# Performance work log

Hardware: AMD Instinct MI355X
Metric: run time of the kernel (lower is better)

The kernel has to match this reference:

```python
import jax, jax.numpy as jnp
import numpy as np

B, L = 1024, 64          # sentences, tokens per sentence
V, E = 100000, 300       # vocab, embedding dim
RH, M, NC = 50, 50, 3    # rnn_hidden, mem_dim, num_class
N = B * L                # total tree nodes


def setup_inputs() -> dict:
    key = jax.random.key(0)
    ks = jax.random.split(key, 24)
    rn = lambda k, s, sc=0.05: jax.random.normal(k, s, dtype=jnp.float32) * sc
    # balanced binary dependency tree per sentence: parent(i) = (i-1)//2
    loc = np.arange(L)
    par_loc = np.where(loc == 0, -1, (loc - 1) // 2)
    parent = np.where(par_loc[None, :] < 0, -1,
                      par_loc[None, :] + np.arange(B)[:, None] * L).reshape(-1)
    depth = np.tile(np.floor(np.log2(loc + 1)).astype(np.int64), B)
    tm = np.zeros(L, np.float32); tm[1:4] = 1.0  # 3 aspect-target tokens/sentence
    return {
        "embed_ids": jax.random.randint(ks[0], (B, L), 0, V),
        "parent": jnp.asarray(parent),
        "depth": jnp.asarray(depth),
        "target_mask": jnp.asarray(np.tile(tm, B)),
        "num_levels": 7,
        "embed_table": rn(ks[1], (V, E), 1.0),
        "W_ih_f": rn(ks[2], (4 * RH, E)), "W_hh_f": rn(ks[3], (4 * RH, RH)),
        "b_f": rn(ks[4], (4 * RH,)),
        "W_ih_b": rn(ks[5], (4 * RH, E)), "W_hh_b": rn(ks[6], (4 * RH, RH)),
        "b_b": rn(ks[7], (4 * RH,)),
        "W_iou": rn(ks[8], (3 * M, 2 * RH)),
        "U_iou_w": rn(ks[9], (3 * M, M)), "U_iou_b": rn(ks[10], (3 * M,)),
        "b_iou": jnp.zeros((3 * M,), jnp.float32),
        "U_f_w": rn(ks[11], (M, M)), "U_f_b": rn(ks[12], (M,)),
        "H_w": rn(ks[13], (M, 2 * RH)), "H_b": rn(ks[14], (M,)),
        "C_w": rn(ks[15], (NC, M)), "C_b": rn(ks[16], (NC,)),
    }


def _lstm(x, W_ih, W_hh, b, reverse):
    # x: (B, L, E) -> (B, L, H); PyTorch gate order i, f, g, o
    xg = jnp.einsum('ble,ge->blg', x, W_ih) + b
    H = W_hh.shape[1]
    def step(carry, xt):
        h, c = carry
        g = xt + h @ W_hh.T
        i, f, gg, o = jnp.split(g, 4, axis=-1)
        c = jax.nn.sigmoid(f) * c + jax.nn.sigmoid(i) * jnp.tanh(gg)
        h = jax.nn.sigmoid(o) * jnp.tanh(c)
        return (h, c), h
    z = jnp.zeros((x.shape[0], H), x.dtype)
    _, hs = jax.lax.scan(step, (z, z), jnp.swapaxes(xg, 0, 1), reverse=reverse)
    return jnp.swapaxes(hs, 0, 1)


def reference(embed_ids, parent, depth, target_mask, num_levels, embed_table,
              W_ih_f, W_hh_f, b_f, W_ih_b, W_hh_b, b_b,
              W_iou, U_iou_w, U_iou_b, b_iou, U_f_w, U_f_b,
              H_w, H_b, C_w, C_b):
    # --- BiLSTM encoder (dropout = identity at inference) ---
    emb = embed_table[embed_ids]                       # (B,L,E) gather
    hf = _lstm(emb, W_ih_f, W_hh_f, b_f, False)
    hb = _lstm(emb, W_ih_b, W_hh_b, b_b, True)
    x = jnp.concatenate([hf, hb], -1).reshape(N, 2 * RH)
    # --- ChildSum TreeLSTM, topological (deepest level first) ---
    iou0 = x @ W_iou.T                                 # (N, 3M)
    h_init = x @ H_w.T + H_b                           # (N, M)
    parent_safe = jnp.where(parent >= 0, parent, N)    # roots -> dummy slot N
    counts = jnp.zeros(N + 1, jnp.int32).at[parent_safe].add(1)
    has_children = (counts[:N] > 0)[:, None]
    h_fin = h_init
    c_fin = jnp.zeros((N, M), jnp.float32)
    h_sum = jnp.zeros((N + 1, M), jnp.float32)         # sum of child h
    fc_sum = jnp.zeros((N + 1, M), jnp.float32)        # sum of f * child c
    for lvl in range(num_levels - 1, -1, -1):
        m = (depth == lvl)[:, None]
        # reduce: leaves never get U_iou bias (no mailbox in DGL)
        iou = iou0 + jnp.where(has_children, h_sum[:N] @ U_iou_w.T + U_iou_b, 0.0) + b_iou
        i, o, u = jnp.split(iou, 3, axis=-1)
        c_new = jax.nn.sigmoid(i) * jnp.tanh(u) + fc_sum[:N]
        h_new = h_init + jax.nn.sigmoid(o) * jnp.tanh(c_new)
        h_fin = jnp.where(m, h_new, h_fin)
        c_fin = jnp.where(m, c_new, c_fin)
        # scatter messages from this level's nodes to their parents
        f = jax.nn.sigmoid(h_new @ U_f_w.T + U_f_b)
        h_sum = h_sum.at[parent_safe].add(jnp.where(m, h_new, 0.0))
        fc_sum = fc_sum.at[parent_safe].add(jnp.where(m, f * c_new, 0.0))
    # --- masked mean pool over target tokens per sentence ---
    tm = target_mask.reshape(B, L)
    pooled = (h_fin.reshape(B, L, M) * tm[:, :, None]).sum(1) / tm.sum(1, keepdims=True)
    logits = pooled @ C_w.T + C_b
    return logits, pooled
```

## Files before the change

### kernel.cpp

```cpp
#include <hip/hip_runtime.h>


typedef __attribute__((ext_vector_type(8))) short bf16x8;
typedef __attribute__((ext_vector_type(4))) float f32x4;

__device__ __forceinline__ float fsig2(float x) {
    float e = __builtin_amdgcn_exp2f(-1.4426950408889634f * x);
    return __builtin_amdgcn_rcpf(1.0f + e);
}
__device__ __forceinline__ float ftanh2(float x) {
    float e = __builtin_amdgcn_exp2f(2.8853900817779268f * x);
    return 1.0f - 2.0f * __builtin_amdgcn_rcpf(1.0f + e);
}

__device__ __forceinline__ unsigned short rne_bf16(float f) {
    unsigned u = __builtin_bit_cast(unsigned, f);
    unsigned r = u + 0x7fffu + ((u >> 16) & 1u);
    return (unsigned short)(r >> 16);
}
__device__ __forceinline__ void split2(float f, unsigned short& h, unsigned short& l) {
    h = rne_bf16(f);
    float fh = __builtin_bit_cast(float, ((unsigned)h) << 16);
    float r = f - fh;
    l = rne_bf16(r);
}

__device__ __forceinline__ void async_lds16(const void* g, void* l) {
    __builtin_amdgcn_global_load_lds(
        (const __attribute__((address_space(1))) unsigned int*)g,
        (__attribute__((address_space(3))) unsigned int*)l, 16, 0, 0);
}

__device__ __forceinline__ bf16x8 pack8(const unsigned short* h) {
    bf16x8 v;
    #pragma unroll
    for (int e = 0; e < 8; ++e) v[e] = (short)h[e];
    return v;
}

__device__ __forceinline__ void conv_item(int q, const float* __restrict__ B1,
                                          const float* __restrict__ B2,
                                          int split, int K, int Rreal, int BN,
                                          unsigned short* __restrict__ out) {
    int n  = q % BN;
    int kq = (q / BN) & 3;
    int c  = q / (BN * 4);
    const float* row = (n < split) ? (B1 + (size_t)n * K) : (B2 + (size_t)(n - split) * K);
    unsigned short h[8], l[8];
    #pragma unroll
    for (int e = 0; e < 8; ++e) {
        int k = c * 32 + kq * 8 + e;
        float v = (n < Rreal && k < K) ? row[k] : 0.0f;
        split2(v, h[e], l[e]);
    }
    size_t hb = ((((size_t)c * 2 + 0) * 4 + kq) * BN + n) * 8;
    size_t lb = ((((size_t)c * 2 + 1) * 4 + kq) * BN + n) * 8;
    *(ushort4*)&out[hb]     = make_ushort4(h[0], h[1], h[2], h[3]);
    *(ushort4*)&out[hb + 4] = make_ushort4(h[4], h[5], h[6], h[7]);
    *(ushort4*)&out[lb]     = make_ushort4(l[0], l[1], l[2], l[3]);
    *(ushort4*)&out[lb + 4] = make_ushort4(l[4], l[5], l[6], l[7]);
}

constexpr int WHC_DIR = 2 * 2 * 4 * 208 * 8;

__global__ void conv_fused(const float* __restrict__ Wihf, const float* __restrict__ Wihb,
                           const float* __restrict__ Wiou, const float* __restrict__ Hw,
                           const float* __restrict__ Whhf, const float* __restrict__ Whhb,
                           unsigned short* __restrict__ B1c,
                           unsigned short* __restrict__ B3c,
                           unsigned short* __restrict__ Whc) {
    int q = blockIdx.x * 256 + threadIdx.x;
    if (q < 17920) {
        conv_item(q, Wihf, Wihb, 200, 300, 400, 448, B1c);
    } else if (q < 22016) {
        conv_item(q - 17920, Wiou, Hw, 150, 100, 200, 256, B3c);
    } else if (q < 23680) {
        conv_item(q - 22016, Whhf, Whhf, 200, 50, 200, 208, Whc);
    } else if (q < 25344) {
        conv_item(q - 23680, Whhb, Whhb, 200, 50, 200, 208, Whc + WHC_DIR);
    }
}

template<int BN, int KCH, int KREAL, int NCOLS, bool GATHER>
__global__ __launch_bounds__(256)
void gemm_split(const float* __restrict__ A, const int* __restrict__ ids,
                const unsigned short* __restrict__ Bc,
                const float* __restrict__ bias1, const float* __restrict__ bias2,
                int split, float* __restrict__ C) {
    constexpr int NTW = BN / 64;
    __shared__ __align__(16) unsigned short As[2 * 4 * 64 * 8];
    __shared__ __align__(16) unsigned short Bt[64 * BN];

    const int tid = threadIdx.x;
    const int m0 = blockIdx.x * 64;
    const int w = tid >> 6, lane = tid & 63;
    const int r16 = lane & 15, quad = lane >> 4;
    const int wn = w * (BN / 4);

    const int mA = tid & 63, kqA = tid >> 6;
    const float* arow = GATHER ? (A + (size_t)ids[m0 + mA] * KREAL)
                               : (A + (size_t)(m0 + mA) * KREAL);

    float ar[8];
    {
        int k0 = kqA * 8;
        if (k0 + 8 <= KREAL) {
            float4 p = *(const float4*)(arow + k0);
            float4 q = *(const float4*)(arow + k0 + 4);
            ar[0]=p.x; ar[1]=p.y; ar[2]=p.z; ar[3]=p.w;
            ar[4]=q.x; ar[5]=q.y; ar[6]=q.z; ar[7]=q.w;
        } else {
            #pragma unroll
            for (int e = 0; e < 8; ++e) ar[e] = (k0 + e < KREAL) ? arow[k0 + e] : 0.0f;
        }
    }

    f32x4 acc[4][NTW] = {};

    for (int c = 0; c < KCH; ++c) {
        __syncthreads();
        {
            const unsigned short* src = Bc + (size_t)c * 64 * BN + tid * 8;
            #pragma unroll
            for (int i = 0; i < BN / 32; ++i)
                async_lds16(src + (size_t)i * 2048, Bt + i * 2048 + tid * 8);
        }
        {
            unsigned short h[8], l[8];
            #pragma unroll
            for (int e = 0; e < 8; ++e) split2(ar[e], h[e], l[e]);
            *(bf16x8*)&As[((0 * 4 + kqA) * 64 + mA) * 8] = pack8(h);
            *(bf16x8*)&As[((1 * 4 + kqA) * 64 + mA) * 8] = pack8(l);
        }
        __syncthreads();
        if (c + 1 < KCH) {
            int k0 = (c + 1) * 32 + kqA * 8;
            if (k0 + 8 <= KREAL) {
                float4 p = *(const float4*)(arow + k0);
                float4 q = *(const float4*)(arow + k0 + 4);
                ar[0]=p.x; ar[1]=p.y; ar[2]=p.z; ar[3]=p.w;
                ar[4]=q.x; ar[5]=q.y; ar[6]=q.z; ar[7]=q.w;
            } else {
                #pragma unroll
                for (int e = 0; e < 8; ++e) ar[e] = (k0 + e < KREAL) ? arow[k0 + e] : 0.0f;
            }
        }
        bf16x8 af[2][4];
        #pragma unroll
        for (int i = 0; i < 4; ++i) {
            af[0][i] = *(const bf16x8*)&As[((0 * 4 + quad) * 64 + i * 16 + r16) * 8];
            af[1][i] = *(const bf16x8*)&As[((1 * 4 + quad) * 64 + i * 16 + r16) * 8];
        }
        #pragma unroll
        for (int t = 0; t < NTW; ++t) {
            bf16x8 bh = *(const bf16x8*)&Bt[((0 * 4 + quad) * BN + wn + t * 16 + r16) * 8];
            bf16x8 bl = *(const bf16x8*)&Bt[((1 * 4 + quad) * BN + wn + t * 16 + r16) * 8];
            #pragma unroll
            for (int i = 0; i < 4; ++i) {
                acc[i][t] = __builtin_amdgcn_mfma_f32_16x16x32_bf16(af[0][i], bh, acc[i][t], 0, 0, 0);
                acc[i][t] = __builtin_amdgcn_mfma_f32_16x16x32_bf16(af[1][i], bh, acc[i][t], 0, 0, 0);
                acc[i][t] = __builtin_amdgcn_mfma_f32_16x16x32_bf16(af[0][i], bl, acc[i][t], 0, 0, 0);
            }
        }
    }

    #pragma unroll
    for (int t = 0; t < NTW; ++t) {
        int ncol = wn + t * 16 + r16;
        if (ncol < NCOLS) {
            float bv = (ncol < split) ? bias1[ncol] : bias2[ncol - split];
            #pragma unroll
            for (int i = 0; i < 4; ++i)
                #pragma unroll
                for (int r = 0; r < 4; ++r) {
                    int mrow = m0 + i * 16 + quad * 4 + r;
                    C[(size_t)mrow * NCOLS + ncol] = acc[i][t][r] + bv;
                }
        }
    }
}

__global__ __launch_bounds__(256)
void lstm_mfma(const float* __restrict__ xg, const unsigned short* __restrict__ Whc,
               float* __restrict__ x) {
    const int bi = blockIdx.x;
    const int dir = bi & 1;
    const int b0 = (bi >> 1) * 8;
    const int tid = threadIdx.x;
    const int w = tid >> 6, lane = tid & 63;
    const int r16 = lane & 15, quad = lane >> 4;

    __shared__ __align__(16) unsigned short Ah[8 * 16 * 8];
    __shared__ __align__(16) unsigned short Al[8 * 16 * 8];
    __shared__ __align__(16) float G[208 * 20];
    __shared__ __align__(16) float Xs[3][8][268];

    const int n0 = (w == 0) ? 0 : (w == 1) ? 4 : (w == 2) ? 7 : 10;
    const int nc = (w == 0) ? 4 : 3;

    const unsigned short* Wd = Whc + (size_t)dir * WHC_DIR;
    bf16x8 bfr[4][2][2];
    #pragma unroll
    for (int t = 0; t < 4; ++t) {
        int col = (n0 + ((t < nc) ? t : 0)) * 16 + r16;
        #pragma unroll
        for (int c = 0; c < 2; ++c)
            #pragma unroll
            for (int h = 0; h < 2; ++h)
                bfr[t][c][h] = *(const bf16x8*)&Wd[((((size_t)c * 2 + h) * 4 + quad) * 208 + col) * 8];
    }

    for (int q = tid; q < 512; q += 256) {
        ((unsigned*)Ah)[q] = 0u;
        ((unsigned*)Al)[q] = 0u;
    }

    int ss[2], ms[2];
    bool act[2];
    #pragma unroll
    for (int j = 0; j < 2; ++j) {
        int q = w * 100 + lane + 64 * j;
        ss[j] = q & 7;
        ms[j] = q >> 3;
        act[j] = (lane + 64 * j) < 100;
    }
    float c_reg[2] = {0.0f, 0.0f};

    #pragma unroll
    for (int p = 0; p < 2; ++p) {
        int idx0 = dir ? (63 - p) : p;
        #pragma unroll
        for (int i = 0; i < 2; ++i) {
            int s = w * 2 + i;
            const float* src = xg + ((size_t)(b0 + s) * 64 + idx0) * 400 + dir * 200 + lane * 4;
            async_lds16(src, &Xs[p][s][lane * 4]);
        }
    }
    __syncthreads();

    for (int step = 0; step < 64; ++step) {
        const int buf = step % 3;
        const int idx = dir ? (63 - step) : step;
        {
            int stepn = step + 2; if (stepn > 63) stepn = 63;
            const int slot = (step + 2) % 3;
            const int idxn = dir ? (63 - stepn) : stepn;
            #pragma unroll
            for (int i = 0; i < 2; ++i) {
                int s = w * 2 + i;
                const float* src = xg + ((size_t)(b0 + s) * 64 + idxn) * 400 + dir * 200 + lane * 4;
                async_lds16(src, &Xs[slot][s][lane * 4]);
            }
            __builtin_amdgcn_sched_barrier(0);
        }
        bf16x8 ah[2], al[2];
        #pragma unroll
        for (int c = 0; c < 2; ++c) {
            ah[c] = *(const bf16x8*)&Ah[((c * 4 + quad) * 16 + r16) * 8];
            al[c] = *(const bf16x8*)&Al[((c * 4 + quad) * 16 + r16) * 8];
        }
        f32x4 acc[4] = {};
        #pragma unroll
        for (int t = 0; t < 4; ++t) {
            if (t < nc) {
                #pragma unroll
                for (int c = 0; c < 2; ++c) {
                    acc[t] = __builtin_amdgcn_mfma_f32_16x16x32_bf16(ah[c], bfr[t][c][0], acc[t], 0, 0, 0);
                    acc[t] = __builtin_amdgcn_mfma_f32_16x16x32_bf16(al[c], bfr[t][c][0], acc[t], 0, 0, 0);
                    acc[t] = __builtin_amdgcn_mfma_f32_16x16x32_bf16(ah[c], bfr[t][c][1], acc[t], 0, 0, 0);
                }
            }
        }
        #pragma unroll
        for (int t = 0; t < 4; ++t) {
            if (t < nc) {
                int col = (n0 + t) * 16 + r16;
                *(f32x4*)&G[col * 20 + quad * 4] = acc[t];
            }
        }
        asm volatile("s_waitcnt lgkmcnt(0) vmcnt(8)" ::: "memory");
        __builtin_amdgcn_sched_barrier(0);
        __builtin_amdgcn_s_barrier();
        __builtin_amdgcn_sched_barrier(0);
        #pragma unroll
        for (int j = 0; j < 2; ++j) {
            if (act[j]) {
                int s = ss[j], m = ms[j];
                float gi = G[m * 20 + s]         + Xs[buf][s][m];
                float gf = G[(m + 50) * 20 + s]  + Xs[buf][s][m + 50];
                float gg = G[(m + 100) * 20 + s] + Xs[buf][s][m + 100];
                float go = G[(m + 150) * 20 + s] + Xs[buf][s][m + 150];
                c_reg[j] = fsig2(gf) * c_reg[j] + fsig2(gi) * ftanh2(gg);
                float h = fsig2(go) * ftanh2(c_reg[j]);
                unsigned short hh, hl;
                split2(h, hh, hl);
                Ah[(m >> 3) * 128 + s * 8 + (m & 7)] = hh;
                Al[(m >> 3) * 128 + s * 8 + (m & 7)] = hl;
                x[((size_t)(b0 + s) * 64 + idx) * 100 + dir * 50 + m] = h;
            }
        }
        asm volatile("s_waitcnt lgkmcnt(0)" ::: "memory");
        __builtin_amdgcn_sched_barrier(0);
        __builtin_amdgcn_s_barrier();
        __builtin_amdgcn_sched_barrier(0);
    }
}

__global__ __launch_bounds__(256)
void tree_kernel(const float* __restrict__ C2,
                 const float* __restrict__ Uw, const float* __restrict__ Ub,
                 const float* __restrict__ Fw, const float* __restrict__ Fb,
                 const float* __restrict__ tmask,
                 const float* __restrict__ Cw, const float* __restrict__ Cb,
                 float* __restrict__ out) {
    const int tid = threadIdx.x;
    const int w = tid >> 6, lane = tid & 63;
    const int s = blockIdx.x * 4 + w;

    __shared__ __align__(16) float Us[150][52];
    __shared__ __align__(16) float Fs[50][52];
    __shared__ __align__(16) float HS[4][32][52];
    __shared__ __align__(16) float FC[4][32][52];
    __shared__ __align__(16) float HV[4][64];
    __shared__ __align__(16) float TMS[4][64];

    for (int q = tid; q < 7500; q += 256) Us[q / 50][q % 50] = Uw[q];
    for (int q = tid; q < 2500; q += 256) Fs[q / 50][q % 50] = Fw[q];
    for (int q = tid; q < 4 * 32 * 52; q += 256) {
        int ww = q / (32 * 52), r = q - ww * (32 * 52);
        HS[ww][r / 52][r % 52] = 0.0f;
        FC[ww][r / 52][r % 52] = 0.0f;
    }
    TMS[w][lane] = tmask[(size_t)s * 64 + lane];
    __syncthreads();

    const bool act = lane < 50;
    const int m = act ? lane : 49;
    const float ub0 = Ub[m], ub1 = Ub[50 + m], ub2 = Ub[100 + m];
    const float fb = Fb[m];
    const float* c2s = C2 + (size_t)s * 64 * 200;

    float pr = 0.0f;
    float pc0, pc1, pc2, pc3;
    {
        const float* nb = c2s + 63 * 200;
        pc0 = nb[m]; pc1 = nb[50 + m]; pc2 = nb[100 + m]; pc3 = nb[150 + m];
    }

    for (int l = 6; l >= 0; --l) {
        const int lo = (1 << l) - 1;
        const int hi = min((1 << (l + 1)) - 2, 63);
        for (int loc = lo; loc <= hi; ++loc) {
            const int nxt = (loc < hi) ? (loc + 1) : ((l > 0) ? ((1 << (l - 1)) - 1) : loc);
            float nc0, nc1, nc2, nc3;
            {
                const float* nb = c2s + (size_t)nxt * 200;
                nc0 = nb[m]; nc1 = nb[50 + m]; nc2 = nb[100 + m]; nc3 = nb[150 + m];
            }
            const bool hasch = (loc <= 31);
            float mi = 0.0f, mo = 0.0f, mu = 0.0f, fcv = 0.0f;
            if (hasch) {
                const float* hs = &HS[w][loc][0];
                const float* u0 = &Us[m][0];
                const float* u1 = &Us[50 + m][0];
                const float* u2 = &Us[100 + m][0];
                float i0=0,i1=0,i2=0,i3=0, o0=0,o1=0,o2=0,o3=0, g0=0,g1=0,g2=0,g3=0;
                #pragma unroll
                for (int j = 0; j < 12; ++j) {
                    float4 h4 = *(const float4*)&hs[j * 4];
                    float4 a4 = *(const float4*)&u0[j * 4];
                    float4 b4 = *(const float4*)&u1[j * 4];
                    float4 c4 = *(const float4*)&u2[j * 4];
                    i0 += a4.x*h4.x; i1 += a4.y*h4.y; i2 += a4.z*h4.z; i3 += a4.w*h4.w;
                    o0 += b4.x*h4.x; o1 += b4.y*h4.y; o2 += b4.z*h4.z; o3 += b4.w*h4.w;
                    g0 += c4.x*h4.x; g1 += c4.y*h4.y; g2 += c4.z*h4.z; g3 += c4.w*h4.w;
                }
                float h48 = hs[48], h49 = hs[49];
                mi = ub0 + (i0 + i1) + (i2 + i3) + u0[48]*h48 + u0[49]*h49;
                mo = ub1 + (o0 + o1) + (o2 + o3) + u1[48]*h48 + u1[49]*h49;
                mu = ub2 + (g0 + g1) + (g2 + g3) + u2[48]*h48 + u2[49]*h49;
                fcv = FC[w][loc][m];
            }
            float ig = pc0 + mi, og = pc1 + mo, ug = pc2 + mu;
            float cn = fsig2(ig) * ftanh2(ug) + fcv;
            float hn = pc3 + fsig2(og) * ftanh2(cn);
            pr += TMS[w][loc] * hn;
            if (act) HV[w][lane] = hn;
            {
                const float* hv = &HV[w][0];
                const float* f0 = &Fs[m][0];
                float a0 = 0, a1 = 0, a2 = 0, a3 = 0;
                #pragma unroll
                for (int j = 0; j < 12; ++j) {
                    float4 h4 = *(const float4*)&hv[j * 4];
                    float4 f4 = *(const float4*)&f0[j * 4];
                    a0 += f4.x*h4.x; a1 += f4.y*h4.y; a2 += f4.z*h4.z; a3 += f4.w*h4.w;
                }
                float facc = fb + (a0 + a1) + (a2 + a3) + f0[48]*hv[48] + f0[49]*hv[49];
                if (act && loc > 0) {
                    int p = (loc - 1) >> 1;
                    float fm = fsig2(facc) * cn;
                    HS[w][p][lane] += hn;
                    FC[w][p][lane] += fm;
                }
            }
            pc0 = nc0; pc1 = nc1; pc2 = nc2; pc3 = nc3;
        }
    }

    float ws = 0.0f;
    #pragma unroll
    for (int j = 0; j < 16; ++j) {
        float4 t4 = *(const float4*)&TMS[w][j * 4];
        ws += (t4.x + t4.y) + (t4.z + t4.w);
    }
    float p = pr / ws;
    if (act) {
        out[3072 + (size_t)s * 50 + lane] = p;
        HV[w][lane] = p;
    }
    if (lane < 3) {
        float acc = Cb[lane];
        const float* crow = Cw + lane * 50;
        for (int k = 0; k < 50; ++k) acc += crow[k] * HV[w][k];
        out[(size_t)s * 3 + lane] = acc;
    }
}

extern "C" void kernel_launch(void* const* d_in, const int* in_sizes, int n_in,
                              void* d_out, int out_size, void* d_ws, size_t ws_size,
                              hipStream_t stream) {
    (void)in_sizes; (void)n_in; (void)out_size; (void)ws_size;
    const int*   ids   = (const int*)d_in[0];
    const float* tmask = (const float*)d_in[3];
    const float* table = (const float*)d_in[5];
    const float* Wihf  = (const float*)d_in[6];
    const float* Whhf  = (const float*)d_in[7];
    const float* bf    = (const float*)d_in[8];
    const float* Wihb  = (const float*)d_in[9];
    const float* Whhb  = (const float*)d_in[10];
    const float* bb    = (const float*)d_in[11];
    const float* Wiou  = (const float*)d_in[12];
    const float* Uiouw = (const float*)d_in[13];
    const float* Uioub = (const float*)d_in[14];
    const float* biou  = (const float*)d_in[15];
    const float* Ufw   = (const float*)d_in[16];
    const float* Ufb   = (const float*)d_in[17];
    const float* Hw    = (const float*)d_in[18];
    const float* Hb    = (const float*)d_in[19];
    const float* Cw    = (const float*)d_in[20];
    const float* Cb    = (const float*)d_in[21];
    float* out = (float*)d_out;

    float* wsf = (float*)d_ws;
    float* xg = wsf;
    float* x  = wsf + (size_t)65536 * 400;
    float* C2 = wsf;
    unsigned short* B1c = (unsigned short*)(wsf + 32768000);
    unsigned short* B3c = (unsigned short*)(wsf + 32911360);
    unsigned short* Whc = (unsigned short*)(wsf + 32944128);

    conv_fused<<<99, 256, 0, stream>>>(Wihf, Wihb, Wiou, Hw, Whhf, Whhb,
                                       B1c, B3c, Whc);
    gemm_split<448, 10, 300, 400, true><<<1024, 256, 0, stream>>>(
        table, ids, B1c, bf, bb, 200, xg);
    lstm_mfma<<<256, 256, 0, stream>>>(xg, Whc, x);
    gemm_split<256, 4, 100, 200, false><<<1024, 256, 0, stream>>>(
        x, nullptr, B3c, biou, Hb, 150, C2);
    tree_kernel<<<256, 256, 0, stream>>>(
        C2, Uiouw, Uioub, Ufw, Ufb, tmask, Cw, Cb, out);
}
```

Baseline: 418.6 us.

## Double-buffer A and B LDS tiles in split-bf16 GEMM with one barrier per chunk

Replaces the single-buffered K loop in the split-bf16 MFMA GEMM with a double-buffered pipeline. The async B-tile copy for chunk c+1 and the A global loads two chunks ahead are issued before the MFMAs for chunk c, leaving one barrier per iteration. Tail handling becomes a clamped float4 load with a masked fixup that assumes KREAL%8==4. The aim is to hide global and LDS staging latency behind MFMA work. The cost is doubled LDS use (about 57KB for BN=448), which can lower occupancy, plus redundant clamped loads past the last chunk.

```diff
diff --git a/kernel.cpp b/kernel.cpp
--- a/kernel.cpp
+++ b/kernel.cpp
@@ -83,13 +83,17 @@
 
 template<int BN, int KCH, int KREAL, int NCOLS, bool GATHER>
 __global__ __launch_bounds__(256)
-void gemm_split(const float* __restrict__ A, const int* __restrict__ ids,
-                const unsigned short* __restrict__ Bc,
-                const float* __restrict__ bias1, const float* __restrict__ bias2,
-                int split, float* __restrict__ C) {
+void gemm_db(const float* __restrict__ A, const int* __restrict__ ids,
+             const unsigned short* __restrict__ Bc,
+             const float* __restrict__ bias1, const float* __restrict__ bias2,
+             int split, float* __restrict__ C) {
+    static_assert(KREAL % 8 == 4, "tail fixup assumes KREAL%8==4");
+    static_assert(KCH % 2 == 0, "paired bodies");
     constexpr int NTW = BN / 64;
-    __shared__ __align__(16) unsigned short As[2 * 4 * 64 * 8];
-    __shared__ __align__(16) unsigned short Bt[64 * BN];
+    constexpr int CHB = 64 * BN;
+    constexpr int DMA_PT = BN / 32;
+    __shared__ __align__(16) unsigned short As[2][2 * 4 * 64 * 8];
+    __shared__ __align__(16) unsigned short Bt[2][CHB];
 
     const int tid = threadIdx.x;
     const int m0 = blockIdx.x * 64;
@@ -101,60 +105,59 @@
     const float* arow = GATHER ? (A + (size_t)ids[m0 + mA] * KREAL)
                                : (A + (size_t)(m0 + mA) * KREAL);
 
-    float ar[8];
-    {
-        int k0 = kqA * 8;
-        if (k0 + 8 <= KREAL) {
-            float4 p = *(const float4*)(arow + k0);
-            float4 q = *(const float4*)(arow + k0 + 4);
+    auto stageB = [&](int c, int slot) {
+        int cc = (c < KCH) ? c : (KCH - 1);
+        const unsigned short* src = Bc + (size_t)cc * CHB + tid * 8;
+        unsigned short* dst = &Bt[slot][tid * 8];
+        #pragma unroll
+        for (int i = 0; i < DMA_PT; ++i)
+            async_lds16(src + (size_t)i * 2048, dst + i * 2048);
+    };
+    auto issueA = [&](int c, float4& p, float4& q) {
+        int cc = (c < KCH) ? c : (KCH - 1);
+        int k0 = cc * 32 + kqA * 8;
+        const float* src = arow + ((k0 <= KREAL - 8) ? k0 : (KREAL - 8));
+        p = *(const float4*)src;
+        q = *(const float4*)(src + 4);
+    };
+    auto asWrite = [&](int c, float4 p, float4 q) {
+        float ar[8];
+        int k0 = c * 32 + kqA * 8;
+        if (k0 <= KREAL - 8) {
             ar[0]=p.x; ar[1]=p.y; ar[2]=p.z; ar[3]=p.w;
             ar[4]=q.x; ar[5]=q.y; ar[6]=q.z; ar[7]=q.w;
         } else {
-            #pragma unroll
-            for (int e = 0; e < 8; ++e) ar[e] = (k0 + e < KREAL) ? arow[k0 + e] : 0.0f;
-        }
-    }
+            ar[0] = (k0 + 0 < KREAL) ? q.x : 0.0f;
+            ar[1] = (k0 + 1 < KREAL) ? q.y : 0.0f;
+            ar[2] = (k0 + 2 < KREAL) ? q.z : 0.0f;
+            ar[3] = (k0 + 3 < KREAL) ? q.w : 0.0f;
+            ar[4] = 0.0f; ar[5] = 0.0f; ar[6] = 0.0f; ar[7] = 0.0f;
+        }
+        unsigned short h[8], l[8];
+        #pragma unroll
+        for (int e = 0; e < 8; ++e) split2(ar[e], h[e], l[e]);
+        *(bf16x8*)&As[c & 1][((0 * 4 + kqA) * 64 + mA) * 8] = pack8(h);
+        *(bf16x8*)&As[c & 1][((1 * 4 + kqA) * 64 + mA) * 8] = pack8(l);
+    };
 
     f32x4 acc[4][NTW] = {};
 
-    for (int c = 0; c < KCH; ++c) {
-        __syncthreads();
-        {
-            const unsigned short* src = Bc + (size_t)c * 64 * BN + tid * 8;
-            #pragma unroll
-            for (int i = 0; i < BN / 32; ++i)
-                async_lds16(src + (size_t)i * 2048, Bt + i * 2048 + tid * 8);
-        }
-        {
-            unsigned short h[8], l[8];
-            #pragma unroll
-            for (int e = 0; e < 8; ++e) split2(ar[e], h[e], l[e]);
-            *(bf16x8*)&As[((0 * 4 + kqA) * 64 + mA) * 8] = pack8(h);
-            *(bf16x8*)&As[((1 * 4 + kqA) * 64 + mA) * 8] = pack8(l);
-        }
-        __syncthreads();
-        if (c + 1 < KCH) {
-            int k0 = (c + 1) * 32 + kqA * 8;
-            if (k0 + 8 <= KREAL) {
-                float4 p = *(const float4*)(arow + k0);
-                float4 q = *(const float4*)(arow + k0 + 4);
-                ar[0]=p.x; ar[1]=p.y; ar[2]=p.z; ar[3]=p.w;
-                ar[4]=q.x; ar[5]=q.y; ar[6]=q.z; ar[7]=q.w;
-            } else {
-                #pragma unroll
-                for (int e = 0; e < 8; ++e) ar[e] = (k0 + e < KREAL) ? arow[k0 + e] : 0.0f;
-            }
-        }
+    auto body = [&](int c, float4& wrP, float4& wrQ, float4& ldP, float4& ldQ) {
+        stageB(c + 1, (c + 1) & 1);
+        __builtin_amdgcn_sched_barrier(0);
+        issueA(c + 2, ldP, ldQ);
+        __builtin_amdgcn_sched_barrier(0);
+        asWrite(c + 1, wrP, wrQ);
         bf16x8 af[2][4];
         #pragma unroll
         for (int i = 0; i < 4; ++i) {
-            af[0][i] = *(const bf16x8*)&As[((0 * 4 + quad) * 64 + i * 16 + r16) * 8];
-            af[1][i] = *(const bf16x8*)&As[((1 * 4 + quad) * 64 + i * 16 + r16) * 8];
+            af[0][i] = *(const bf16x8*)&As[c & 1][((0 * 4 + quad) * 64 + i * 16 + r16) * 8];
+            af[1][i] = *(const bf16x8*)&As[c & 1][((1 * 4 + quad) * 64 + i * 16 + r16) * 8];
         }
         #pragma unroll
         for (int t = 0; t < NTW; ++t) {
-            bf16x8 bh = *(const bf16x8*)&Bt[((0 * 4 + quad) * BN + wn + t * 16 + r16) * 8];
-            bf16x8 bl = *(const bf16x8*)&Bt[((1 * 4 + quad) * BN + wn + t * 16 + r16) * 8];
+            bf16x8 bh = *(const bf16x8*)&Bt[c & 1][((0 * 4 + quad) * BN + wn + t * 16 + r16) * 8];
+            bf16x8 bl = *(const bf16x8*)&Bt[c & 1][((1 * 4 + quad) * BN + wn + t * 16 + r16) * 8];
             #pragma unroll
             for (int i = 0; i < 4; ++i) {
                 acc[i][t] = __builtin_amdgcn_mfma_f32_16x16x32_bf16(af[0][i], bh, acc[i][t], 0, 0, 0);
@@ -162,6 +165,25 @@
                 acc[i][t] = __builtin_amdgcn_mfma_f32_16x16x32_bf16(af[0][i], bl, acc[i][t], 0, 0, 0);
             }
         }
+        asm volatile("s_waitcnt lgkmcnt(0) vmcnt(2)" ::: "memory");
+        __builtin_amdgcn_sched_barrier(0);
+        __builtin_amdgcn_s_barrier();
+        __builtin_amdgcn_sched_barrier(0);
+    };
+
+    float4 pA, qA, pB, qB;
+    stageB(0, 0);
+    __builtin_amdgcn_sched_barrier(0);
+    issueA(0, pA, qA);
+    issueA(1, pB, qB);
+    __syncthreads();
+    asWrite(0, pA, qA);
+    __syncthreads();
+
+    #pragma unroll 1
+    for (int c2 = 0; c2 < KCH / 2; ++c2) {
+        body(2 * c2,     pB, qB, pA, qA);
+        body(2 * c2 + 1, pA, qA, pB, qB);
     }
 
     #pragma unroll
@@ -462,10 +484,10 @@
 
     conv_fused<<<99, 256, 0, stream>>>(Wihf, Wihb, Wiou, Hw, Whhf, Whhb,
                                        B1c, B3c, Whc);
-    gemm_split<448, 10, 300, 400, true><<<1024, 256, 0, stream>>>(
+    gemm_db<448, 10, 300, 400, true><<<1024, 256, 0, stream>>>(
         table, ids, B1c, bf, bb, 200, xg);
     lstm_mfma<<<256, 256, 0, stream>>>(xg, Whc, x);
-    gemm_split<256, 4, 100, 200, false><<<1024, 256, 0, stream>>>(
+    gemm_db<256, 4, 100, 200, false><<<1024, 256, 0, stream>>>(
         x, nullptr, B3c, biou, Hb, 150, C2);
     tree_kernel<<<256, 256, 0, stream>>>(
         C2, Uiouw, Uioub, Ufw, Ufb, tmask, Cw, Cb, out);
```

New measurement: 462.2 us. 1.1x slower.

## Pre-gather and split embeddings into MFMA layout before input-projection GEMM

Applied to the files above, without the earlier changes.

Adds a gather_conv kernel that gathers embedding rows by token id, splits them into bf16 hi/lo pairs, and writes them in the tiled layout the MFMA GEMM reads. A new gemm_pre kernel then streams those pre-split A tiles into LDS with async copies, double-buffered. The aim is to take the irregular gather and fp32-to-bf16 split out of the GEMM's inner loop. In exchange it writes and rereads an extra large workspace buffer and adds a kernel launch, and it only runs when the workspace is big enough.

```diff
diff --git a/kernel.cpp b/kernel.cpp
--- a/kernel.cpp
+++ b/kernel.cpp
@@ -78,6 +78,139 @@
         conv_item(q - 22016, Whhf, Whhf, 200, 50, 200, 208, Whc);
     } else if (q < 25344) {
         conv_item(q - 23680, Whhb, Whhb, 200, 50, 200, 208, Whc + WHC_DIR);
+    }
+}
+
+__global__ __launch_bounds__(256)
+void gather_conv(const float* __restrict__ table, const int* __restrict__ ids,
+                 unsigned short* __restrict__ Ac) {
+    __shared__ __align__(16) float L[32][301];
+    __shared__ int rid[32];
+    const int b = blockIdx.x;
+    const int tid = threadIdx.x;
+    if (tid < 32) rid[tid] = ids[b * 32 + tid];
+    __syncthreads();
+    for (int it = tid; it < 2400; it += 256) {
+        int rl = it / 75, j = it - rl * 75;
+        const float* src = table + (size_t)rid[rl] * 300 + j * 4;
+        *(float4*)&L[rl][j * 4] = *(const float4*)src;
+    }
+    __syncthreads();
+    const int b64 = b >> 1;
+    const int rbase = (b & 1) * 32;
+    for (int it = tid; it < 1280; it += 256) {
+        int ck = it >> 5, rl = it & 31;
+        int c = ck >> 2, kq = ck & 3;
+        int k0 = c * 32 + kq * 8;
+        unsigned short h[8], l[8];
+        #pragma unroll
+        for (int e = 0; e < 8; ++e) {
+            int k = k0 + e;
+            float v = (k < 300) ? L[rl][k] : 0.0f;
+            split2(v, h[e], l[e]);
+        }
+        int r = rbase + rl;
+        size_t base = ((size_t)b64 * 10 + c) * 4096;
+        size_t oh = base + (size_t)((0 * 4 + kq) * 64 + r) * 8;
+        size_t ol = base + (size_t)((1 * 4 + kq) * 64 + r) * 8;
+        *(ushort4*)&Ac[oh]     = make_ushort4(h[0], h[1], h[2], h[3]);
+        *(ushort4*)&Ac[oh + 4] = make_ushort4(h[4], h[5], h[6], h[7]);
+        *(ushort4*)&Ac[ol]     = make_ushort4(l[0], l[1], l[2], l[3]);
+        *(ushort4*)&Ac[ol + 4] = make_ushort4(l[4], l[5], l[6], l[7]);
+    }
+}
+
+template<int BN, int KCH, int NCOLS>
+__global__ __launch_bounds__(256, 2)
+void gemm_pre(const unsigned short* __restrict__ Ac,
+              const unsigned short* __restrict__ Bc,
+              const float* __restrict__ bias1, const float* __restrict__ bias2,
+              int split, float* __restrict__ C) {
+    constexpr int NTW = BN / 64;
+    constexpr int CHB = 64 * BN;
+    constexpr int DMA_B = BN / 32;
+    __shared__ __align__(16) unsigned short As[2][4096];
+    __shared__ __align__(16) unsigned short Bt[CHB];
+
+    const int tid = threadIdx.x;
+    const int w = tid >> 6, lane = tid & 63;
+    const int r16 = lane & 15, quad = lane >> 4;
+    const int wn = w * (BN / 4);
+    const unsigned short* Abase = Ac + (size_t)blockIdx.x * (KCH * 4096);
+
+    auto stageB = [&](int c) {
+        int cc = (c < KCH) ? c : (KCH - 1);
+        const unsigned short* src = Bc + (size_t)cc * CHB + tid * 8;
+        unsigned short* dst = &Bt[tid * 8];
+        #pragma unroll
+        for (int i = 0; i < DMA_B; ++i)
+            async_lds16(src + (size_t)i * 2048, dst + i * 2048);
+    };
+    auto stageA = [&](int c, int slot) {
+        int cc = (c < KCH) ? c : (KCH - 1);
+        const unsigned short* src = Abase + (size_t)cc * 4096 + tid * 8;
+        async_lds16(src, &As[slot][tid * 8]);
+        async_lds16(src + 2048, &As[slot][tid * 8 + 2048]);
+    };
+
+    f32x4 acc[4][NTW] = {};
+
+    stageB(0);
+    __builtin_amdgcn_sched_barrier(0);
+    stageA(0, 0);
+    __builtin_amdgcn_sched_barrier(0);
+
+    #pragma unroll 1
+    for (int c = 0; c < KCH; ++c) {
+        asm volatile("s_waitcnt vmcnt(0)" ::: "memory");
+        __builtin_amdgcn_sched_barrier(0);
+        __builtin_amdgcn_s_barrier();
+        __builtin_amdgcn_sched_barrier(0);
+        bf16x8 bh[NTW], bl[NTW];
+        #pragma unroll
+        for (int t = 0; t < NTW; ++t) {
+            bh[t] = *(const bf16x8*)&Bt[((0 * 4 + quad) * BN + wn + t * 16 + r16) * 8];
+            bl[t] = *(const bf16x8*)&Bt[((1 * 4 + quad) * BN + wn + t * 16 + r16) * 8];
+        }
+        asm volatile("s_waitcnt lgkmcnt(0)" ::: "memory");
+        __builtin_amdgcn_sched_barrier(0);
+        __builtin_amdgcn_s_barrier();
+        __builtin_amdgcn_sched_barrier(0);
+        stageB(c + 1);
+        __builtin_amdgcn_sched_barrier(0);
+        stageA(c + 1, (c + 1) & 1);
+        __builtin_amdgcn_sched_barrier(0);
+        bf16x8 af[2][4];
+        #pragma unroll
+        for (int i = 0; i < 4; ++i) {
+            af[0][i] = *(const bf16x8*)&As[c & 1][((0 * 4 + quad) * 64 + i * 16 + r16) * 8];
+            af[1][i] = *(const bf16x8*)&As[c & 1][((1 * 4 + quad) * 64 + i * 16 + r16) * 8];
+        }
+        #pragma unroll
+        for (int t = 0; t < NTW; ++t) {
+            #pragma unroll
+            for (int i = 0; i < 4; ++i) {
+                acc[i][t] = __builtin_amdgcn_mfma_f32_16x16x32_bf16(af[0][i], bh[t], acc[i][t], 0, 0, 0);
+                acc[i][t] = __builtin_amdgcn_mfma_f32_16x16x32_bf16(af[1][i], bh[t], acc[i][t], 0, 0, 0);
+                acc[i][t] = __builtin_amdgcn_mfma_f32_16x16x32_bf16(af[0][i], bl[t], acc[i][t], 0, 0, 0);
+            }
+        }
+    }
+
+    const int m0 = blockIdx.x * 64;
+    #pragma unroll
+    for (int t = 0; t < NTW; ++t) {
+        int ncol = wn + t * 16 + r16;
+        if (ncol < NCOLS) {
+            float bv = (ncol < split) ? bias1[ncol] : bias2[ncol - split];
+            #pragma unroll
+            for (int i = 0; i < 4; ++i)
+                #pragma unroll
+                for (int r = 0; r < 4; ++r) {
+                    int mrow = m0 + i * 16 + quad * 4 + r;
+                    C[(size_t)mrow * NCOLS + ncol] = acc[i][t][r] + bv;
+                }
+        }
     }
 }
 
@@ -430,7 +563,7 @@
 extern "C" void kernel_launch(void* const* d_in, const int* in_sizes, int n_in,
                               void* d_out, int out_size, void* d_ws, size_t ws_size,
                               hipStream_t stream) {
-    (void)in_sizes; (void)n_in; (void)out_size; (void)ws_size;
+    (void)in_sizes; (void)n_in; (void)out_size;
     const int*   ids   = (const int*)d_in[0];
     const float* tmask = (const float*)d_in[3];
     const float* table = (const float*)d_in[5];
@@ -459,11 +592,20 @@
     unsigned short* B1c = (unsigned short*)(wsf + 32768000);
     unsigned short* B3c = (unsigned short*)(wsf + 32911360);
     unsigned short* Whc = (unsigned short*)(wsf + 32944128);
+    unsigned short* Ac  = (unsigned short*)(wsf + 33000000);
+    const size_t ws_need = ((size_t)33000000 + 20971520) * 4;
+    const bool big_ws = (ws_size >= ws_need);
 
     conv_fused<<<99, 256, 0, stream>>>(Wihf, Wihb, Wiou, Hw, Whhf, Whhb,
                                        B1c, B3c, Whc);
-    gemm_split<448, 10, 300, 400, true><<<1024, 256, 0, stream>>>(
-        table, ids, B1c, bf, bb, 200, xg);
+    if (big_ws) {
+        gather_conv<<<2048, 256, 0, stream>>>(table, ids, Ac);
+        gemm_pre<448, 10, 400><<<1024, 256, 0, stream>>>(
+            Ac, B1c, bf, bb, 200, xg);
+    } else {
+        gemm_split<448, 10, 300, 400, true><<<1024, 256, 0, stream>>>(
+            table, ids, B1c, bf, bb, 200, xg);
+    }
     lstm_mfma<<<256, 256, 0, stream>>>(xg, Whc, x);
     gemm_split<256, 4, 100, 200, false><<<1024, 256, 0, stream>>>(
         x, nullptr, B3c, biou, Hb, 150, C2);
```

Result: slower. 441.2 us (+5.4%).
